# Kernel optimization log

Measured on AMD Instinct MI355X. Metric: run time of the kernel, lower is better.

## Reference

```python
import jax, jax.numpy as jnp
import numpy as np

B, S, D, H = 2, 2048, 1024, 16
HD = D // H  # 64
NUM_BUCKETS = 32
MAX_DISTANCE = 128


def _relative_position_bucket(relative_position, num_buckets=NUM_BUCKETS, max_distance=MAX_DISTANCE):
    # bidirectional=True branch of the torch code
    num_buckets //= 2
    rel_buckets = (relative_position > 0).astype(jnp.int32) * num_buckets
    rp = jnp.abs(relative_position)
    max_exact = num_buckets // 2
    is_small = rp < max_exact
    # log-spaced buckets for larger distances
    rp_large = max_exact + (
        jnp.log(rp.astype(jnp.float32) / max_exact)
        / np.log(max_distance / max_exact)
        * (num_buckets - max_exact)
    ).astype(jnp.int32)
    rp_large = jnp.minimum(rp_large, num_buckets - 1)
    return rel_buckets + jnp.where(is_small, rp, rp_large)


def compute_bias(rel_bias, query_length, key_length):
    ctx = jnp.arange(query_length)[:, None]
    mem = jnp.arange(key_length)[None, :]
    buckets = _relative_position_bucket(mem - ctx)  # [q, k]
    values = rel_bias[buckets]                      # [q, k, h]
    return jnp.transpose(values, (2, 0, 1))[None]   # [1, h, q, k]


def setup_inputs() -> dict:
    key = jax.random.key(0)
    ks = jax.random.split(key, 6)
    scale = 1.0 / np.sqrt(D)
    return {
        "hidden_states": jax.random.normal(ks[0], (B, S, D), jnp.float32),
        "mask": jnp.ones((B, 1, 1, S), jnp.int32),
        "Wq": jax.random.normal(ks[1], (D, D), jnp.float32) * scale,
        "Wk": jax.random.normal(ks[2], (D, D), jnp.float32) * scale,
        "Wv": jax.random.normal(ks[3], (D, D), jnp.float32) * scale,
        "Wo": jax.random.normal(ks[4], (D, D), jnp.float32) * scale,
        "rel_bias": jax.random.normal(ks[5], (NUM_BUCKETS, H), jnp.float32),
    }


def reference(hidden_states, mask, Wq, Wk, Wv, Wo, rel_bias):
    b, s, _ = hidden_states.shape
    # projections (no bias), split heads -> [b, h, s, hd]
    def proj(x, W):
        return jnp.einsum("bsd,ed->bse", x, W).reshape(b, s, H, HD).transpose(0, 2, 1, 3)
    q = proj(hidden_states, Wq)
    k = proj(hidden_states, Wk)
    v = proj(hidden_states, Wv)
    # unscaled attention scores (T5 style): [b, h, s, s]
    scores = jnp.einsum("bhqd,bhkd->bhqk", q, k)
    position_bias = compute_bias(rel_bias, s, s)
    scores = scores + position_bias
    scores = jnp.where(mask == 0, jnp.float32(-1e9), scores)
    attn_weights = jax.nn.softmax(scores, axis=-1)
    # dropout p=0.0 (eval): identity
    attn_output = jnp.einsum("bhqk,bhkd->bhqd", attn_weights, v)
    attn_output = attn_output.transpose(0, 2, 1, 3).reshape(b, s, H * HD)
    attn_output = jnp.einsum("bse,de->bsd", attn_output, Wo)
    return attn_output, attn_weights, position_bias
```

## Files before the change

### kernel.cpp

```cpp
#include <hip/hip_runtime.h>

typedef __attribute__((ext_vector_type(8))) _Float16 half8;
typedef __attribute__((ext_vector_type(4))) _Float16 half4;
typedef __attribute__((ext_vector_type(4))) float f32x4;

#define SEQ 2048
#define DMODEL 1024
#define NHEAD 16
#define HEADD 64
#define NBH 32
#define LUTW 4096

__device__ __forceinline__ void nt_store_f4(float* p, f32x4 v) {
    __builtin_nontemporal_store(v, (f32x4*)p);
}

#define LDS_BAR() do {                                   \
    __builtin_amdgcn_sched_barrier(0);                   \
    asm volatile("s_waitcnt lgkmcnt(0)" ::: "memory");   \
    __builtin_amdgcn_sched_barrier(0);                   \
    __builtin_amdgcn_s_barrier();                        \
    __builtin_amdgcn_sched_barrier(0);                   \
} while (0)

__device__ __forceinline__ int rel_bucket(int rel) {
    int ret = (rel > 0) ? 16 : 0;
    int rp = rel < 0 ? -rel : rel;
    if (rp < 8) return ret + rp;
    float x = logf((float)rp * 0.125f) / 2.7725887f * 8.0f;
    int v = 8 + (int)x;
    v = v < 15 ? v : 15;
    return ret + v;
}

__global__ __launch_bounds__(256) void prep_kernel(const float* __restrict__ hs,
                                                   const float* __restrict__ Wq,
                                                   const float* __restrict__ Wk,
                                                   const float* __restrict__ Wv,
                                                   const float* __restrict__ Wo,
                                                   const float* __restrict__ rel_bias,
                                                   _Float16* __restrict__ Xh,
                                                   _Float16* __restrict__ Wqh,
                                                   _Float16* __restrict__ Wkh,
                                                   _Float16* __restrict__ Wvh,
                                                   _Float16* __restrict__ Woh,
                                                   float* __restrict__ lut) {
    int bid = blockIdx.x;
    if (bid < 4096) {
        const float* in;
        _Float16* out;
        int base;
        if (bid < 2048)      { in = hs; out = Xh;  base = bid; }
        else if (bid < 2560) { in = Wq; out = Wqh; base = bid - 2048; }
        else if (bid < 3072) { in = Wk; out = Wkh; base = bid - 2560; }
        else if (bid < 3584) { in = Wv; out = Wvh; base = bid - 3072; }
        else                 { in = Wo; out = Woh; base = bid - 3584; }
        int i = (base * 256 + threadIdx.x) * 8;
        f32x4 a = *(const f32x4*)(in + i);
        f32x4 b = *(const f32x4*)(in + i + 4);
        half8 r;
        r[0] = (_Float16)a[0]; r[1] = (_Float16)a[1];
        r[2] = (_Float16)a[2]; r[3] = (_Float16)a[3];
        r[4] = (_Float16)b[0]; r[5] = (_Float16)b[1];
        r[6] = (_Float16)b[2]; r[7] = (_Float16)b[3];
        *(half8*)(out + i) = r;
    } else {
        int i = (bid - 4096) * 256 + threadIdx.x;
        int h = i >> 12;
        int idx = i & (LUTW - 1);
        int rel = idx - 2047;
        int b = rel_bucket(rel);
        lut[i] = rel_bias[b * NHEAD + h];
    }
}

__global__ __launch_bounds__(256) void proj3_kernel(const _Float16* __restrict__ Xh,
                                                    const _Float16* __restrict__ Wqh,
                                                    const _Float16* __restrict__ Wkh,
                                                    const _Float16* __restrict__ Wvh,
                                                    _Float16* __restrict__ Qh,
                                                    _Float16* __restrict__ Kh,
                                                    _Float16* __restrict__ Vt,
                                                    const float* __restrict__ lut,
                                                    float* __restrict__ posb) {
    int z = blockIdx.z;
    if (z == 3) {
        int flat = blockIdx.y * 8 + blockIdx.x;
        const size_t total = (size_t)NHEAD * SEQ * SEQ / 4;
        for (size_t idx = (size_t)flat * 256 + threadIdx.x; idx < total; idx += 65536) {
            size_t e = idx * 4;
            int k = (int)(e & 2047);
            int q = (int)((e >> 11) & 2047);
            int h = (int)(e >> 22);
            f32x4 v;
            __builtin_memcpy(&v, lut + h * LUTW + (k - q + 2047), 16);
            nt_store_f4(posb + e, v);
        }
        return;
    }
    const _Float16* B = (z == 0) ? Wqh : (z == 1) ? Wkh : Wvh;
    int l = threadIdx.x & 63, w = threadIdx.x >> 6;
    int row0 = blockIdx.y * 128 + (w >> 1) * 64;
    int col0 = blockIdx.x * 128 + (w & 1) * 64;
    int ar = l & 15, ak = (l >> 4) * 8;
    f32x4 acc[4][4] = {};
    for (int k0 = 0; k0 < DMODEL; k0 += 32) {
        half8 af[4], bf[4];
#pragma unroll
        for (int mi = 0; mi < 4; mi++)
            af[mi] = *(const half8*)(Xh + (size_t)(row0 + mi * 16 + ar) * DMODEL + k0 + ak);
#pragma unroll
        for (int ni = 0; ni < 4; ni++)
            bf[ni] = *(const half8*)(B + (size_t)(col0 + ni * 16 + ar) * DMODEL + k0 + ak);
#pragma unroll
        for (int mi = 0; mi < 4; mi++)
#pragma unroll
            for (int ni = 0; ni < 4; ni++)
                acc[mi][ni] = __builtin_amdgcn_mfma_f32_16x16x32_f16(af[mi], bf[ni], acc[mi][ni], 0, 0, 0);
    }
    int cr = (l >> 4) * 4, cc = l & 15;
    if (z < 2) {
        _Float16* C = z == 0 ? Qh : Kh;
#pragma unroll
        for (int mi = 0; mi < 4; mi++)
#pragma unroll
            for (int ni = 0; ni < 4; ni++) {
                int c = col0 + ni * 16 + cc;
#pragma unroll
                for (int j = 0; j < 4; j++)
                    C[(size_t)(row0 + mi * 16 + cr + j) * DMODEL + c] = (_Float16)acc[mi][ni][j];
            }
    } else {
#pragma unroll
        for (int mi = 0; mi < 4; mi++)
#pragma unroll
            for (int ni = 0; ni < 4; ni++) {
                int c = col0 + ni * 16 + cc;
                int h = c >> 6, hd = c & 63;
                int r = row0 + mi * 16 + cr;
                int b = r >> 11, s0 = r & 2047;
                half4 pk;
#pragma unroll
                for (int j = 0; j < 4; j++) pk[j] = (_Float16)acc[mi][ni][j];
                *(half4*)(Vt + (size_t)((b * NHEAD + h) * HEADD + hd) * SEQ + s0) = pk;
            }
    }
}

__global__ __launch_bounds__(256) void outgemm_kernel(const _Float16* __restrict__ A,
                                                      const _Float16* __restrict__ B,
                                                      float* __restrict__ C) {
    int l = threadIdx.x & 63, w = threadIdx.x >> 6;
    int row0 = blockIdx.y * 128 + (w >> 1) * 64;
    int col0 = blockIdx.x * 128 + (w & 1) * 64;
    int ar = l & 15, ak = (l >> 4) * 8;
    f32x4 acc[4][4] = {};
    for (int k0 = 0; k0 < DMODEL; k0 += 32) {
        half8 af[4], bf[4];
#pragma unroll
        for (int mi = 0; mi < 4; mi++)
            af[mi] = *(const half8*)(A + (size_t)(row0 + mi * 16 + ar) * DMODEL + k0 + ak);
#pragma unroll
        for (int ni = 0; ni < 4; ni++)
            bf[ni] = *(const half8*)(B + (size_t)(col0 + ni * 16 + ar) * DMODEL + k0 + ak);
#pragma unroll
        for (int mi = 0; mi < 4; mi++)
#pragma unroll
            for (int ni = 0; ni < 4; ni++)
                acc[mi][ni] = __builtin_amdgcn_mfma_f32_16x16x32_f16(af[mi], bf[ni], acc[mi][ni], 0, 0, 0);
    }
    int cr = (l >> 4) * 4, cc = l & 15;
#pragma unroll
    for (int mi = 0; mi < 4; mi++)
#pragma unroll
        for (int ni = 0; ni < 4; ni++) {
            int c = col0 + ni * 16 + cc;
#pragma unroll
            for (int j = 0; j < 4; j++)
                C[(size_t)(row0 + mi * 16 + cr + j) * DMODEL + c] = acc[mi][ni][j];
        }
}

__global__ __launch_bounds__(256) void attn_kernel(const _Float16* __restrict__ Q,
                                                   const _Float16* __restrict__ Kg,
                                                   const _Float16* __restrict__ Vg,
                                                   const float* __restrict__ lut,
                                                   const int* __restrict__ mask,
                                                   float* __restrict__ wts,
                                                   _Float16* __restrict__ attn0) {
    __shared__ _Float16 Kt[64][68];
    __shared__ _Float16 Vl[64][68];
    __shared__ _Float16 Pl[4][16][72];
    int tid = threadIdx.x;
    int l = tid & 63, w = tid >> 6;
    int bid = blockIdx.x;
    int xcd = bid & 7, idx = bid >> 3;
    int bh = (idx >> 4) * 8 + xcd;
    int qpair = idx & 15;
    int b = bh >> 4, h = bh & 15;
    int qbaseA = qpair * 64 + w * 16;
    int qbaseB = qbaseA + 1024;
    size_t hoff = (size_t)(b * SEQ) * DMODEL + h * HEADD;
    int ar = l & 15, g = l >> 4, ak = g * 8;
    const float* luth = lut + h * LUTW;
    float* ob = wts + (size_t)bh * SEQ * SEQ;
    int qA = qbaseA + ar;
    int qB = qbaseB + ar;

    int sr = tid >> 2, sc = (tid & 3) * 16;
    const _Float16* Ksrc = Kg + hoff + sc;
    const _Float16* Vsrc = Vg + ((size_t)bh * HEADD + sr) * SEQ + sc;

    half8 qfA[2], qfB[2];
#pragma unroll
    for (int kk = 0; kk < 2; kk++) {
        qfA[kk] = *(const half8*)(Q + hoff + (size_t)qA * DMODEL + kk * 32 + ak);
        qfB[kk] = *(const half8*)(Q + hoff + (size_t)qB * DMODEL + kk * 32 + ak);
    }

    half8 s0 = *(const half8*)(Ksrc + (size_t)sr * DMODEL);
    half8 s1 = *(const half8*)(Ksrc + (size_t)sr * DMODEL + 8);
    float mA = -3e38f, lsumA = 0.f;
    for (int k0 = 0; k0 < SEQ; k0 += 64) {
        *(half8*)&Kt[sr][sc] = s0;
        *(half8*)&Kt[sr][sc + 8] = s1;
        LDS_BAR();
        if (k0 + 64 < SEQ) {
            s0 = *(const half8*)(Ksrc + (size_t)(k0 + 64 + sr) * DMODEL);
            s1 = *(const half8*)(Ksrc + (size_t)(k0 + 64 + sr) * DMODEL + 8);
        }
        f32x4 acc[4] = {};
#pragma unroll
        for (int ni = 0; ni < 4; ni++)
#pragma unroll
            for (int kk = 0; kk < 2; kk++) {
                half8 kf = *(const half8*)&Kt[ni * 16 + ar][kk * 32 + ak];
                acc[ni] = __builtin_amdgcn_mfma_f32_16x16x32_f16(kf, qfA[kk], acc[ni], 0, 0, 0);
            }
        LDS_BAR();
        float vv[16];
#pragma unroll
        for (int ni = 0; ni < 4; ni++) {
            int kcol = k0 + ni * 16 + g * 4;
            int4 mk = *(const int4*)(mask + b * SEQ + kcol);
            const int* mp = (const int*)&mk;
            f32x4 lb4;
            __builtin_memcpy(&lb4, luth + kcol - qA + 2047, 16);
#pragma unroll
            for (int j = 0; j < 4; j++)
                vv[ni * 4 + j] = mp[j] ? (acc[ni][j] + lb4[j]) : -1e9f;
        }
        float t8[8];
#pragma unroll
        for (int t = 0; t < 8; t++) t8[t] = fmaxf(vv[t], vv[t + 8]);
        float t4a = fmaxf(t8[0], t8[4]), t4b = fmaxf(t8[1], t8[5]);
        float t4c = fmaxf(t8[2], t8[6]), t4d = fmaxf(t8[3], t8[7]);
        float vmax = fmaxf(fmaxf(t4a, t4b), fmaxf(t4c, t4d));
        float mn = fmaxf(mA, vmax);
        float scale = __expf(mA - mn);
        float e[16];
#pragma unroll
        for (int t = 0; t < 16; t++) e[t] = __expf(vv[t] - mn);
        float s8[8];
#pragma unroll
        for (int t = 0; t < 8; t++) s8[t] = e[t] + e[t + 8];
        float s4a = s8[0] + s8[4], s4b = s8[1] + s8[5];
        float s4c = s8[2] + s8[6], s4d = s8[3] + s8[7];
        lsumA = lsumA * scale + (s4a + s4b) + (s4c + s4d);
        mA = mn;
    }
    half8 t0 = *(const half8*)(Ksrc + (size_t)sr * DMODEL);
    half8 t1 = *(const half8*)(Ksrc + (size_t)sr * DMODEL + 8);
    half8 v0 = *(const half8*)(Vsrc);
    half8 v1 = *(const half8*)(Vsrc + 8);
#pragma unroll
    for (int off2 = 16; off2 <= 32; off2 <<= 1) {
        float mo = __shfl_xor(mA, off2);
        float lo = __shfl_xor(lsumA, off2);
        float mn = fmaxf(mA, mo);
        lsumA = lsumA * __expf(mA - mn) + lo * __expf(mo - mn);
        mA = mn;
    }
    float invlA = 1.0f / lsumA;
    LDS_BAR();

    f32x4 oaccA[4] = {};
    float mB = -3e38f, lsumB = 0.f;
    for (int k0 = 0; k0 < SEQ; k0 += 64) {
        *(half8*)&Kt[sr][sc] = t0;
        *(half8*)&Kt[sr][sc + 8] = t1;
        *(half8*)&Vl[sr][sc] = v0;
        *(half8*)&Vl[sr][sc + 8] = v1;
        LDS_BAR();
        if (k0 + 64 < SEQ) {
            t0 = *(const half8*)(Ksrc + (size_t)(k0 + 64 + sr) * DMODEL);
            t1 = *(const half8*)(Ksrc + (size_t)(k0 + 64 + sr) * DMODEL + 8);
            v0 = *(const half8*)(Vsrc + k0 + 64);
            v1 = *(const half8*)(Vsrc + k0 + 64 + 8);
        }
        f32x4 accA[4] = {}, accB[4] = {};
#pragma unroll
        for (int ni = 0; ni < 4; ni++)
#pragma unroll
            for (int kk = 0; kk < 2; kk++) {
                half8 kf = *(const half8*)&Kt[ni * 16 + ar][kk * 32 + ak];
                accA[ni] = __builtin_amdgcn_mfma_f32_16x16x32_f16(kf, qfA[kk], accA[ni], 0, 0, 0);
                accB[ni] = __builtin_amdgcn_mfma_f32_16x16x32_f16(kf, qfB[kk], accB[ni], 0, 0, 0);
            }
#pragma unroll
        for (int ni = 0; ni < 4; ni++) {
            int kcol = k0 + ni * 16 + g * 4;
            int4 mk = *(const int4*)(mask + b * SEQ + kcol);
            const int* mp = (const int*)&mk;
            f32x4 lb4;
            __builtin_memcpy(&lb4, luth + kcol - qA + 2047, 16);
            f32x4 wv;
#pragma unroll
            for (int j = 0; j < 4; j++) {
                float v = mp[j] ? (accA[ni][j] + lb4[j]) : -1e9f;
                wv[j] = __expf(v - mA) * invlA;
            }
            nt_store_f4(ob + (size_t)qA * SEQ + kcol, wv);
            half4 ph;
#pragma unroll
            for (int j = 0; j < 4; j++) ph[j] = (_Float16)wv[j];
            *(half4*)&Pl[w][ar][ni * 16 + g * 4] = ph;
        }
#pragma unroll
        for (int kk2 = 0; kk2 < 2; kk2++) {
            half8 pa = *(half8*)&Pl[w][ar][kk2 * 32 + g * 8];
#pragma unroll
            for (int ni = 0; ni < 4; ni++) {
                half8 vf = *(const half8*)&Vl[ni * 16 + ar][kk2 * 32 + g * 8];
                oaccA[ni] = __builtin_amdgcn_mfma_f32_16x16x32_f16(pa, vf, oaccA[ni], 0, 0, 0);
            }
        }
        {
            float vv[16];
#pragma unroll
            for (int ni = 0; ni < 4; ni++) {
                int kcol = k0 + ni * 16 + g * 4;
                int4 mk = *(const int4*)(mask + b * SEQ + kcol);
                const int* mp = (const int*)&mk;
                f32x4 lb4;
                __builtin_memcpy(&lb4, luth + kcol - qB + 2047, 16);
#pragma unroll
                for (int j = 0; j < 4; j++)
                    vv[ni * 4 + j] = mp[j] ? (accB[ni][j] + lb4[j]) : -1e9f;
            }
            float t8[8];
#pragma unroll
            for (int t = 0; t < 8; t++) t8[t] = fmaxf(vv[t], vv[t + 8]);
            float t4a = fmaxf(t8[0], t8[4]), t4b = fmaxf(t8[1], t8[5]);
            float t4c = fmaxf(t8[2], t8[6]), t4d = fmaxf(t8[3], t8[7]);
            float vmax = fmaxf(fmaxf(t4a, t4b), fmaxf(t4c, t4d));
            float mn = fmaxf(mB, vmax);
            float scale = __expf(mB - mn);
            float e[16];
#pragma unroll
            for (int t = 0; t < 16; t++) e[t] = __expf(vv[t] - mn);
            float s8[8];
#pragma unroll
            for (int t = 0; t < 8; t++) s8[t] = e[t] + e[t + 8];
            float s4a = s8[0] + s8[4], s4b = s8[1] + s8[5];
            float s4c = s8[2] + s8[6], s4d = s8[3] + s8[7];
            lsumB = lsumB * scale + (s4a + s4b) + (s4c + s4d);
            mB = mn;
        }
        LDS_BAR();
    }
#pragma unroll
    for (int ni = 0; ni < 4; ni++)
#pragma unroll
        for (int j = 0; j < 4; j++)
            attn0[(size_t)(b * SEQ + qbaseA + g * 4 + j) * DMODEL + h * HEADD + ni * 16 + ar] =
                (_Float16)oaccA[ni][j];
    half8 u0 = *(const half8*)(Ksrc + (size_t)sr * DMODEL);
    half8 u1 = *(const half8*)(Ksrc + (size_t)sr * DMODEL + 8);
    half8 w0 = *(const half8*)(Vsrc);
    half8 w1 = *(const half8*)(Vsrc + 8);
#pragma unroll
    for (int off2 = 16; off2 <= 32; off2 <<= 1) {
        float mo = __shfl_xor(mB, off2);
        float lo = __shfl_xor(lsumB, off2);
        float mn = fmaxf(mB, mo);
        lsumB = lsumB * __expf(mB - mn) + lo * __expf(mo - mn);
        mB = mn;
    }
    float invlB = 1.0f / lsumB;
    LDS_BAR();

    f32x4 oaccB[4] = {};
    for (int k0 = 0; k0 < SEQ; k0 += 64) {
        *(half8*)&Kt[sr][sc] = u0;
        *(half8*)&Kt[sr][sc + 8] = u1;
        *(half8*)&Vl[sr][sc] = w0;
        *(half8*)&Vl[sr][sc + 8] = w1;
        LDS_BAR();
        if (k0 + 64 < SEQ) {
            u0 = *(const half8*)(Ksrc + (size_t)(k0 + 64 + sr) * DMODEL);
            u1 = *(const half8*)(Ksrc + (size_t)(k0 + 64 + sr) * DMODEL + 8);
            w0 = *(const half8*)(Vsrc + k0 + 64);
            w1 = *(const half8*)(Vsrc + k0 + 64 + 8);
        }
        f32x4 acc[4] = {};
#pragma unroll
        for (int ni = 0; ni < 4; ni++)
#pragma unroll
            for (int kk = 0; kk < 2; kk++) {
                half8 kf = *(const half8*)&Kt[ni * 16 + ar][kk * 32 + ak];
                acc[ni] = __builtin_amdgcn_mfma_f32_16x16x32_f16(kf, qfB[kk], acc[ni], 0, 0, 0);
            }
#pragma unroll
        for (int ni = 0; ni < 4; ni++) {
            int kcol = k0 + ni * 16 + g * 4;
            int4 mk = *(const int4*)(mask + b * SEQ + kcol);
            const int* mp = (const int*)&mk;
            f32x4 lb4;
            __builtin_memcpy(&lb4, luth + kcol - qB + 2047, 16);
            f32x4 wv;
#pragma unroll
            for (int j = 0; j < 4; j++) {
                float v = mp[j] ? (acc[ni][j] + lb4[j]) : -1e9f;
                wv[j] = __expf(v - mB) * invlB;
            }
            nt_store_f4(ob + (size_t)qB * SEQ + kcol, wv);
            half4 ph;
#pragma unroll
            for (int j = 0; j < 4; j++) ph[j] = (_Float16)wv[j];
            *(half4*)&Pl[w][ar][ni * 16 + g * 4] = ph;
        }
#pragma unroll
        for (int kk2 = 0; kk2 < 2; kk2++) {
            half8 pa = *(half8*)&Pl[w][ar][kk2 * 32 + g * 8];
#pragma unroll
            for (int ni = 0; ni < 4; ni++) {
                half8 vf = *(const half8*)&Vl[ni * 16 + ar][kk2 * 32 + g * 8];
                oaccB[ni] = __builtin_amdgcn_mfma_f32_16x16x32_f16(pa, vf, oaccB[ni], 0, 0, 0);
            }
        }
        LDS_BAR();
    }
#pragma unroll
    for (int ni = 0; ni < 4; ni++)
#pragma unroll
        for (int j = 0; j < 4; j++)
            attn0[(size_t)(b * SEQ + qbaseB + g * 4 + j) * DMODEL + h * HEADD + ni * 16 + ar] =
                (_Float16)oaccB[ni][j];
}

extern "C" void kernel_launch(void* const* d_in, const int* in_sizes, int n_in,
                              void* d_out, int out_size, void* d_ws, size_t ws_size,
                              hipStream_t stream) {
    const float* hs = (const float*)d_in[0];
    const int* mask = (const int*)d_in[1];
    const float* Wq = (const float*)d_in[2];
    const float* Wk = (const float*)d_in[3];
    const float* Wv = (const float*)d_in[4];
    const float* Wo = (const float*)d_in[5];
    const float* rel_bias = (const float*)d_in[6];

    float* out_attn = (float*)d_out;
    float* out_wts = out_attn + (size_t)2 * SEQ * DMODEL;
    float* out_posb = out_wts + (size_t)NBH * SEQ * SEQ;

    char* ws = (char*)d_ws;
    size_t off = 0;
    auto carve = [&](size_t bytes) { void* p = ws + off; off += (bytes + 255) & ~(size_t)255; return p; };
    _Float16* Xh  = (_Float16*)carve((size_t)2 * SEQ * DMODEL * 2);
    _Float16* Wqh = (_Float16*)carve((size_t)DMODEL * DMODEL * 2);
    _Float16* Wkh = (_Float16*)carve((size_t)DMODEL * DMODEL * 2);
    _Float16* Wvh = (_Float16*)carve((size_t)DMODEL * DMODEL * 2);
    _Float16* Woh = (_Float16*)carve((size_t)DMODEL * DMODEL * 2);
    _Float16* Qh  = (_Float16*)carve((size_t)2 * SEQ * DMODEL * 2);
    _Float16* Kh  = (_Float16*)carve((size_t)2 * SEQ * DMODEL * 2);
    _Float16* Vt  = (_Float16*)carve((size_t)NBH * HEADD * SEQ * 2);
    _Float16* A0h = (_Float16*)carve((size_t)2 * SEQ * DMODEL * 2);
    float* lut    = (float*)carve((size_t)NHEAD * LUTW * 4);

    prep_kernel<<<4352, 256, 0, stream>>>(hs, Wq, Wk, Wv, Wo, rel_bias,
                                          Xh, Wqh, Wkh, Wvh, Woh, lut);

    dim3 pg(DMODEL / 128, (2 * SEQ) / 128, 4);
    proj3_kernel<<<pg, 256, 0, stream>>>(Xh, Wqh, Wkh, Wvh, Qh, Kh, Vt, lut, out_posb);

    attn_kernel<<<512, 256, 0, stream>>>(Qh, Kh, Vt, lut, mask, out_wts, A0h);

    dim3 og(DMODEL / 128, (2 * SEQ) / 128);
    outgemm_kernel<<<og, 256, 0, stream>>>(A0h, Woh, out_attn);
}
```

Measured before the change: 442.7 us.

## Double-buffer K/V tiles in LDS to halve barriers per iteration

The K and V staging tiles become two-slot LDS buffers. Each iteration now computes from the current slot, writes the prefetched next tile into the other slot, and issues a single barrier, where it previously used two. Global prefetch now runs two tiles ahead across all three passes. This cuts barrier stalls per tile at the cost of doubling the K/V LDS footprint, which may lower occupancy.

```diff
diff --git a/kernel.cpp b/kernel.cpp
--- a/kernel.cpp
+++ b/kernel.cpp
@@ -188,8 +188,8 @@
                                                    const int* __restrict__ mask,
                                                    float* __restrict__ wts,
                                                    _Float16* __restrict__ attn0) {
-    __shared__ _Float16 Kt[64][68];
-    __shared__ _Float16 Vl[64][68];
+    __shared__ _Float16 Kb[2][64][68];
+    __shared__ _Float16 Vb[2][64][68];
     __shared__ _Float16 Pl[4][16][72];
     int tid = threadIdx.x;
     int l = tid & 63, w = tid >> 6;
@@ -220,24 +220,22 @@
 
     half8 s0 = *(const half8*)(Ksrc + (size_t)sr * DMODEL);
     half8 s1 = *(const half8*)(Ksrc + (size_t)sr * DMODEL + 8);
+    *(half8*)&Kb[0][sr][sc] = s0;
+    *(half8*)&Kb[0][sr][sc + 8] = s1;
+    s0 = *(const half8*)(Ksrc + (size_t)(64 + sr) * DMODEL);
+    s1 = *(const half8*)(Ksrc + (size_t)(64 + sr) * DMODEL + 8);
+    LDS_BAR();
     float mA = -3e38f, lsumA = 0.f;
     for (int k0 = 0; k0 < SEQ; k0 += 64) {
-        *(half8*)&Kt[sr][sc] = s0;
-        *(half8*)&Kt[sr][sc + 8] = s1;
-        LDS_BAR();
-        if (k0 + 64 < SEQ) {
-            s0 = *(const half8*)(Ksrc + (size_t)(k0 + 64 + sr) * DMODEL);
-            s1 = *(const half8*)(Ksrc + (size_t)(k0 + 64 + sr) * DMODEL + 8);
-        }
+        int cur = (k0 >> 6) & 1;
         f32x4 acc[4] = {};
 #pragma unroll
         for (int ni = 0; ni < 4; ni++)
 #pragma unroll
             for (int kk = 0; kk < 2; kk++) {
-                half8 kf = *(const half8*)&Kt[ni * 16 + ar][kk * 32 + ak];
+                half8 kf = *(const half8*)&Kb[cur][ni * 16 + ar][kk * 32 + ak];
                 acc[ni] = __builtin_amdgcn_mfma_f32_16x16x32_f16(kf, qfA[kk], acc[ni], 0, 0, 0);
             }
-        LDS_BAR();
         float vv[16];
 #pragma unroll
         for (int ni = 0; ni < 4; ni++) {
@@ -268,11 +266,17 @@
         float s4c = s8[2] + s8[6], s4d = s8[3] + s8[7];
         lsumA = lsumA * scale + (s4a + s4b) + (s4c + s4d);
         mA = mn;
-    }
-    half8 t0 = *(const half8*)(Ksrc + (size_t)sr * DMODEL);
-    half8 t1 = *(const half8*)(Ksrc + (size_t)sr * DMODEL + 8);
-    half8 v0 = *(const half8*)(Vsrc);
-    half8 v1 = *(const half8*)(Vsrc + 8);
+        if (k0 + 128 < SEQ) {
+            *(half8*)&Kb[cur ^ 1][sr][sc] = s0;
+            *(half8*)&Kb[cur ^ 1][sr][sc + 8] = s1;
+            s0 = *(const half8*)(Ksrc + (size_t)(k0 + 128 + sr) * DMODEL);
+            s1 = *(const half8*)(Ksrc + (size_t)(k0 + 128 + sr) * DMODEL + 8);
+        } else if (k0 + 64 < SEQ) {
+            *(half8*)&Kb[cur ^ 1][sr][sc] = s0;
+            *(half8*)&Kb[cur ^ 1][sr][sc + 8] = s1;
+        }
+        LDS_BAR();
+    }
 #pragma unroll
     for (int off2 = 16; off2 <= 32; off2 <<= 1) {
         float mo = __shfl_xor(mA, off2);
@@ -282,28 +286,30 @@
         mA = mn;
     }
     float invlA = 1.0f / lsumA;
+
+    half8 t0 = *(const half8*)(Ksrc + (size_t)sr * DMODEL);
+    half8 t1 = *(const half8*)(Ksrc + (size_t)sr * DMODEL + 8);
+    half8 v0 = *(const half8*)(Vsrc);
+    half8 v1 = *(const half8*)(Vsrc + 8);
+    *(half8*)&Kb[0][sr][sc] = t0;
+    *(half8*)&Kb[0][sr][sc + 8] = t1;
+    *(half8*)&Vb[0][sr][sc] = v0;
+    *(half8*)&Vb[0][sr][sc + 8] = v1;
+    t0 = *(const half8*)(Ksrc + (size_t)(64 + sr) * DMODEL);
+    t1 = *(const half8*)(Ksrc + (size_t)(64 + sr) * DMODEL + 8);
+    v0 = *(const half8*)(Vsrc + 64);
+    v1 = *(const half8*)(Vsrc + 64 + 8);
     LDS_BAR();
-
     f32x4 oaccA[4] = {};
     float mB = -3e38f, lsumB = 0.f;
     for (int k0 = 0; k0 < SEQ; k0 += 64) {
-        *(half8*)&Kt[sr][sc] = t0;
-        *(half8*)&Kt[sr][sc + 8] = t1;
-        *(half8*)&Vl[sr][sc] = v0;
-        *(half8*)&Vl[sr][sc + 8] = v1;
-        LDS_BAR();
-        if (k0 + 64 < SEQ) {
-            t0 = *(const half8*)(Ksrc + (size_t)(k0 + 64 + sr) * DMODEL);
-            t1 = *(const half8*)(Ksrc + (size_t)(k0 + 64 + sr) * DMODEL + 8);
-            v0 = *(const half8*)(Vsrc + k0 + 64);
-            v1 = *(const half8*)(Vsrc + k0 + 64 + 8);
-        }
+        int cur = (k0 >> 6) & 1;
         f32x4 accA[4] = {}, accB[4] = {};
 #pragma unroll
         for (int ni = 0; ni < 4; ni++)
 #pragma unroll
             for (int kk = 0; kk < 2; kk++) {
-                half8 kf = *(const half8*)&Kt[ni * 16 + ar][kk * 32 + ak];
+                half8 kf = *(const half8*)&Kb[cur][ni * 16 + ar][kk * 32 + ak];
                 accA[ni] = __builtin_amdgcn_mfma_f32_16x16x32_f16(kf, qfA[kk], accA[ni], 0, 0, 0);
                 accB[ni] = __builtin_amdgcn_mfma_f32_16x16x32_f16(kf, qfB[kk], accB[ni], 0, 0, 0);
             }
@@ -331,7 +337,7 @@
             half8 pa = *(half8*)&Pl[w][ar][kk2 * 32 + g * 8];
 #pragma unroll
             for (int ni = 0; ni < 4; ni++) {
-                half8 vf = *(const half8*)&Vl[ni * 16 + ar][kk2 * 32 + g * 8];
+                half8 vf = *(const half8*)&Vb[cur][ni * 16 + ar][kk2 * 32 + g * 8];
                 oaccA[ni] = __builtin_amdgcn_mfma_f32_16x16x32_f16(pa, vf, oaccA[ni], 0, 0, 0);
             }
         }
@@ -367,6 +373,21 @@
             lsumB = lsumB * scale + (s4a + s4b) + (s4c + s4d);
             mB = mn;
         }
+        if (k0 + 128 < SEQ) {
+            *(half8*)&Kb[cur ^ 1][sr][sc] = t0;
+            *(half8*)&Kb[cur ^ 1][sr][sc + 8] = t1;
+            *(half8*)&Vb[cur ^ 1][sr][sc] = v0;
+            *(half8*)&Vb[cur ^ 1][sr][sc + 8] = v1;
+            t0 = *(const half8*)(Ksrc + (size_t)(k0 + 128 + sr) * DMODEL);
+            t1 = *(const half8*)(Ksrc + (size_t)(k0 + 128 + sr) * DMODEL + 8);
+            v0 = *(const half8*)(Vsrc + k0 + 128);
+            v1 = *(const half8*)(Vsrc + k0 + 128 + 8);
+        } else if (k0 + 64 < SEQ) {
+            *(half8*)&Kb[cur ^ 1][sr][sc] = t0;
+            *(half8*)&Kb[cur ^ 1][sr][sc + 8] = t1;
+            *(half8*)&Vb[cur ^ 1][sr][sc] = v0;
+            *(half8*)&Vb[cur ^ 1][sr][sc + 8] = v1;
+        }
         LDS_BAR();
     }
 #pragma unroll
@@ -375,10 +396,6 @@
         for (int j = 0; j < 4; j++)
             attn0[(size_t)(b * SEQ + qbaseA + g * 4 + j) * DMODEL + h * HEADD + ni * 16 + ar] =
                 (_Float16)oaccA[ni][j];
-    half8 u0 = *(const half8*)(Ksrc + (size_t)sr * DMODEL);
-    half8 u1 = *(const half8*)(Ksrc + (size_t)sr * DMODEL + 8);
-    half8 w0 = *(const half8*)(Vsrc);
-    half8 w1 = *(const half8*)(Vsrc + 8);
 #pragma unroll
     for (int off2 = 16; off2 <= 32; off2 <<= 1) {
         float mo = __shfl_xor(mB, off2);
@@ -388,27 +405,29 @@
         mB = mn;
     }
     float invlB = 1.0f / lsumB;
+
+    half8 u0 = *(const half8*)(Ksrc + (size_t)sr * DMODEL);
+    half8 u1 = *(const half8*)(Ksrc + (size_t)sr * DMODEL + 8);
+    half8 w0 = *(const half8*)(Vsrc);
+    half8 w1 = *(const half8*)(Vsrc + 8);
+    *(half8*)&Kb[0][sr][sc] = u0;
+    *(half8*)&Kb[0][sr][sc + 8] = u1;
+    *(half8*)&Vb[0][sr][sc] = w0;
+    *(half8*)&Vb[0][sr][sc + 8] = w1;
+    u0 = *(const half8*)(Ksrc + (size_t)(64 + sr) * DMODEL);
+    u1 = *(const half8*)(Ksrc + (size_t)(64 + sr) * DMODEL + 8);
+    w0 = *(const half8*)(Vsrc + 64);
+    w1 = *(const half8*)(Vsrc + 64 + 8);
     LDS_BAR();
-
     f32x4 oaccB[4] = {};
     for (int k0 = 0; k0 < SEQ; k0 += 64) {
-        *(half8*)&Kt[sr][sc] = u0;
-        *(half8*)&Kt[sr][sc + 8] = u1;
-        *(half8*)&Vl[sr][sc] = w0;
-        *(half8*)&Vl[sr][sc + 8] = w1;
-        LDS_BAR();
-        if (k0 + 64 < SEQ) {
-            u0 = *(const half8*)(Ksrc + (size_t)(k0 + 64 + sr) * DMODEL);
-            u1 = *(const half8*)(Ksrc + (size_t)(k0 + 64 + sr) * DMODEL + 8);
-            w0 = *(const half8*)(Vsrc + k0 + 64);
-            w1 = *(const half8*)(Vsrc + k0 + 64 + 8);
-        }
+        int cur = (k0 >> 6) & 1;
         f32x4 acc[4] = {};
 #pragma unroll
         for (int ni = 0; ni < 4; ni++)
 #pragma unroll
             for (int kk = 0; kk < 2; kk++) {
-                half8 kf = *(const half8*)&Kt[ni * 16 + ar][kk * 32 + ak];
+                half8 kf = *(const half8*)&Kb[cur][ni * 16 + ar][kk * 32 + ak];
                 acc[ni] = __builtin_amdgcn_mfma_f32_16x16x32_f16(kf, qfB[kk], acc[ni], 0, 0, 0);
             }
 #pragma unroll
@@ -435,9 +454,24 @@
             half8 pa = *(half8*)&Pl[w][ar][kk2 * 32 + g * 8];
 #pragma unroll
             for (int ni = 0; ni < 4; ni++) {
-                half8 vf = *(const half8*)&Vl[ni * 16 + ar][kk2 * 32 + g * 8];
+                half8 vf = *(const half8*)&Vb[cur][ni * 16 + ar][kk2 * 32 + g * 8];
                 oaccB[ni] = __builtin_amdgcn_mfma_f32_16x16x32_f16(pa, vf, oaccB[ni], 0, 0, 0);
             }
+        }
+        if (k0 + 128 < SEQ) {
+            *(half8*)&Kb[cur ^ 1][sr][sc] = u0;
+            *(half8*)&Kb[cur ^ 1][sr][sc + 8] = u1;
+            *(half8*)&Vb[cur ^ 1][sr][sc] = w0;
+            *(half8*)&Vb[cur ^ 1][sr][sc + 8] = w1;
+            u0 = *(const half8*)(Ksrc + (size_t)(k0 + 128 + sr) * DMODEL);
+            u1 = *(const half8*)(Ksrc + (size_t)(k0 + 128 + sr) * DMODEL + 8);
+            w0 = *(const half8*)(Vsrc + k0 + 128);
+            w1 = *(const half8*)(Vsrc + k0 + 128 + 8);
+        } else if (k0 + 64 < SEQ) {
+            *(half8*)&Kb[cur ^ 1][sr][sc] = u0;
+            *(half8*)&Kb[cur ^ 1][sr][sc + 8] = u1;
+            *(half8*)&Vb[cur ^ 1][sr][sc] = w0;
+            *(half8*)&Vb[cur ^ 1][sr][sc + 8] = w1;
         }
         LDS_BAR();
     }
```

Measured after the change: 447.5 us. No clear change (+1.1%).

## Merge row-stat passes for both query tiles, drop third K/V sweep

Applied to the files above, without the earlier changes.

The first K sweep now computes the running softmax max and sum for both query tiles A and B at once, with the cross-lane reductions done together. The second sweep then writes normalized weights and accumulates P·V for both tiles, so the separate third sweep over K/V for tile B is removed. This cuts one full pass of K/V global loads, LDS staging and barriers per block. In exchange, two output accumulator sets and more softmax state stay live at the same time, which raises register pressure and may lower occupancy.

```diff
diff --git a/kernel.cpp b/kernel.cpp
--- a/kernel.cpp
+++ b/kernel.cpp
@@ -221,6 +221,7 @@
     half8 s0 = *(const half8*)(Ksrc + (size_t)sr * DMODEL);
     half8 s1 = *(const half8*)(Ksrc + (size_t)sr * DMODEL + 8);
     float mA = -3e38f, lsumA = 0.f;
+    float mB = -3e38f, lsumB = 0.f;
     for (int k0 = 0; k0 < SEQ; k0 += 64) {
         *(half8*)&Kt[sr][sc] = s0;
         *(half8*)&Kt[sr][sc + 8] = s1;
@@ -229,45 +230,80 @@
             s0 = *(const half8*)(Ksrc + (size_t)(k0 + 64 + sr) * DMODEL);
             s1 = *(const half8*)(Ksrc + (size_t)(k0 + 64 + sr) * DMODEL + 8);
         }
-        f32x4 acc[4] = {};
+        f32x4 accA[4] = {}, accB[4] = {};
 #pragma unroll
         for (int ni = 0; ni < 4; ni++)
 #pragma unroll
             for (int kk = 0; kk < 2; kk++) {
                 half8 kf = *(const half8*)&Kt[ni * 16 + ar][kk * 32 + ak];
-                acc[ni] = __builtin_amdgcn_mfma_f32_16x16x32_f16(kf, qfA[kk], acc[ni], 0, 0, 0);
+                accA[ni] = __builtin_amdgcn_mfma_f32_16x16x32_f16(kf, qfA[kk], accA[ni], 0, 0, 0);
+                accB[ni] = __builtin_amdgcn_mfma_f32_16x16x32_f16(kf, qfB[kk], accB[ni], 0, 0, 0);
             }
         LDS_BAR();
-        float vv[16];
-#pragma unroll
-        for (int ni = 0; ni < 4; ni++) {
-            int kcol = k0 + ni * 16 + g * 4;
-            int4 mk = *(const int4*)(mask + b * SEQ + kcol);
-            const int* mp = (const int*)&mk;
-            f32x4 lb4;
-            __builtin_memcpy(&lb4, luth + kcol - qA + 2047, 16);
-#pragma unroll
-            for (int j = 0; j < 4; j++)
-                vv[ni * 4 + j] = mp[j] ? (acc[ni][j] + lb4[j]) : -1e9f;
-        }
-        float t8[8];
-#pragma unroll
-        for (int t = 0; t < 8; t++) t8[t] = fmaxf(vv[t], vv[t + 8]);
-        float t4a = fmaxf(t8[0], t8[4]), t4b = fmaxf(t8[1], t8[5]);
-        float t4c = fmaxf(t8[2], t8[6]), t4d = fmaxf(t8[3], t8[7]);
-        float vmax = fmaxf(fmaxf(t4a, t4b), fmaxf(t4c, t4d));
-        float mn = fmaxf(mA, vmax);
-        float scale = __expf(mA - mn);
-        float e[16];
-#pragma unroll
-        for (int t = 0; t < 16; t++) e[t] = __expf(vv[t] - mn);
-        float s8[8];
-#pragma unroll
-        for (int t = 0; t < 8; t++) s8[t] = e[t] + e[t + 8];
-        float s4a = s8[0] + s8[4], s4b = s8[1] + s8[5];
-        float s4c = s8[2] + s8[6], s4d = s8[3] + s8[7];
-        lsumA = lsumA * scale + (s4a + s4b) + (s4c + s4d);
-        mA = mn;
+        {
+            float vv[16];
+#pragma unroll
+            for (int ni = 0; ni < 4; ni++) {
+                int kcol = k0 + ni * 16 + g * 4;
+                int4 mk = *(const int4*)(mask + b * SEQ + kcol);
+                const int* mp = (const int*)&mk;
+                f32x4 lb4;
+                __builtin_memcpy(&lb4, luth + kcol - qA + 2047, 16);
+#pragma unroll
+                for (int j = 0; j < 4; j++)
+                    vv[ni * 4 + j] = mp[j] ? (accA[ni][j] + lb4[j]) : -1e9f;
+            }
+            float t8[8];
+#pragma unroll
+            for (int t = 0; t < 8; t++) t8[t] = fmaxf(vv[t], vv[t + 8]);
+            float t4a = fmaxf(t8[0], t8[4]), t4b = fmaxf(t8[1], t8[5]);
+            float t4c = fmaxf(t8[2], t8[6]), t4d = fmaxf(t8[3], t8[7]);
+            float vmax = fmaxf(fmaxf(t4a, t4b), fmaxf(t4c, t4d));
+            float mn = fmaxf(mA, vmax);
+            float scale = __expf(mA - mn);
+            float e[16];
+#pragma unroll
+            for (int t = 0; t < 16; t++) e[t] = __expf(vv[t] - mn);
+            float s8[8];
+#pragma unroll
+            for (int t = 0; t < 8; t++) s8[t] = e[t] + e[t + 8];
+            float s4a = s8[0] + s8[4], s4b = s8[1] + s8[5];
+            float s4c = s8[2] + s8[6], s4d = s8[3] + s8[7];
+            lsumA = lsumA * scale + (s4a + s4b) + (s4c + s4d);
+            mA = mn;
+        }
+        {
+            float vv[16];
+#pragma unroll
+            for (int ni = 0; ni < 4; ni++) {
+                int kcol = k0 + ni * 16 + g * 4;
+                int4 mk = *(const int4*)(mask + b * SEQ + kcol);
+                const int* mp = (const int*)&mk;
+                f32x4 lb4;
+                __builtin_memcpy(&lb4, luth + kcol - qB + 2047, 16);
+#pragma unroll
+                for (int j = 0; j < 4; j++)
+                    vv[ni * 4 + j] = mp[j] ? (accB[ni][j] + lb4[j]) : -1e9f;
+            }
+            float t8[8];
+#pragma unroll
+            for (int t = 0; t < 8; t++) t8[t] = fmaxf(vv[t], vv[t + 8]);
+            float t4a = fmaxf(t8[0], t8[4]), t4b = fmaxf(t8[1], t8[5]);
+            float t4c = fmaxf(t8[2], t8[6]), t4d = fmaxf(t8[3], t8[7]);
+            float vmax = fmaxf(fmaxf(t4a, t4b), fmaxf(t4c, t4d));
+            float mn = fmaxf(mB, vmax);
+            float scale = __expf(mB - mn);
+            float e[16];
+#pragma unroll
+            for (int t = 0; t < 16; t++) e[t] = __expf(vv[t] - mn);
+            float s8[8];
+#pragma unroll
+            for (int t = 0; t < 8; t++) s8[t] = e[t] + e[t + 8];
+            float s4a = s8[0] + s8[4], s4b = s8[1] + s8[5];
+            float s4c = s8[2] + s8[6], s4d = s8[3] + s8[7];
+            lsumB = lsumB * scale + (s4a + s4b) + (s4c + s4d);
+            mB = mn;
+        }
     }
     half8 t0 = *(const half8*)(Ksrc + (size_t)sr * DMODEL);
     half8 t1 = *(const half8*)(Ksrc + (size_t)sr * DMODEL + 8);
@@ -280,12 +316,17 @@
         float mn = fmaxf(mA, mo);
         lsumA = lsumA * __expf(mA - mn) + lo * __expf(mo - mn);
         mA = mn;
+        mo = __shfl_xor(mB, off2);
+        lo = __shfl_xor(lsumB, off2);
+        mn = fmaxf(mB, mo);
+        lsumB = lsumB * __expf(mB - mn) + lo * __expf(mo - mn);
+        mB = mn;
     }
     float invlA = 1.0f / lsumA;
+    float invlB = 1.0f / lsumB;
     LDS_BAR();
 
-    f32x4 oaccA[4] = {};
-    float mB = -3e38f, lsumB = 0.f;
+    f32x4 oaccA[4] = {}, oaccB[4] = {};
     for (int k0 = 0; k0 < SEQ; k0 += 64) {
         *(half8*)&Kt[sr][sc] = t0;
         *(half8*)&Kt[sr][sc + 8] = t1;
@@ -335,82 +376,6 @@
                 oaccA[ni] = __builtin_amdgcn_mfma_f32_16x16x32_f16(pa, vf, oaccA[ni], 0, 0, 0);
             }
         }
-        {
-            float vv[16];
-#pragma unroll
-            for (int ni = 0; ni < 4; ni++) {
-                int kcol = k0 + ni * 16 + g * 4;
-                int4 mk = *(const int4*)(mask + b * SEQ + kcol);
-                const int* mp = (const int*)&mk;
-                f32x4 lb4;
-                __builtin_memcpy(&lb4, luth + kcol - qB + 2047, 16);
-#pragma unroll
-                for (int j = 0; j < 4; j++)
-                    vv[ni * 4 + j] = mp[j] ? (accB[ni][j] + lb4[j]) : -1e9f;
-            }
-            float t8[8];
-#pragma unroll
-            for (int t = 0; t < 8; t++) t8[t] = fmaxf(vv[t], vv[t + 8]);
-            float t4a = fmaxf(t8[0], t8[4]), t4b = fmaxf(t8[1], t8[5]);
-            float t4c = fmaxf(t8[2], t8[6]), t4d = fmaxf(t8[3], t8[7]);
-            float vmax = fmaxf(fmaxf(t4a, t4b), fmaxf(t4c, t4d));
-            float mn = fmaxf(mB, vmax);
-            float scale = __expf(mB - mn);
-            float e[16];
-#pragma unroll
-            for (int t = 0; t < 16; t++) e[t] = __expf(vv[t] - mn);
-            float s8[8];
-#pragma unroll
-            for (int t = 0; t < 8; t++) s8[t] = e[t] + e[t + 8];
-            float s4a = s8[0] + s8[4], s4b = s8[1] + s8[5];
-            float s4c = s8[2] + s8[6], s4d = s8[3] + s8[7];
-            lsumB = lsumB * scale + (s4a + s4b) + (s4c + s4d);
-            mB = mn;
-        }
-        LDS_BAR();
-    }
-#pragma unroll
-    for (int ni = 0; ni < 4; ni++)
-#pragma unroll
-        for (int j = 0; j < 4; j++)
-            attn0[(size_t)(b * SEQ + qbaseA + g * 4 + j) * DMODEL + h * HEADD + ni * 16 + ar] =
-                (_Float16)oaccA[ni][j];
-    half8 u0 = *(const half8*)(Ksrc + (size_t)sr * DMODEL);
-    half8 u1 = *(const half8*)(Ksrc + (size_t)sr * DMODEL + 8);
-    half8 w0 = *(const half8*)(Vsrc);
-    half8 w1 = *(const half8*)(Vsrc + 8);
-#pragma unroll
-    for (int off2 = 16; off2 <= 32; off2 <<= 1) {
-        float mo = __shfl_xor(mB, off2);
-        float lo = __shfl_xor(lsumB, off2);
-        float mn = fmaxf(mB, mo);
-        lsumB = lsumB * __expf(mB - mn) + lo * __expf(mo - mn);
-        mB = mn;
-    }
-    float invlB = 1.0f / lsumB;
-    LDS_BAR();
-
-    f32x4 oaccB[4] = {};
-    for (int k0 = 0; k0 < SEQ; k0 += 64) {
-        *(half8*)&Kt[sr][sc] = u0;
-        *(half8*)&Kt[sr][sc + 8] = u1;
-        *(half8*)&Vl[sr][sc] = w0;
-        *(half8*)&Vl[sr][sc + 8] = w1;
-        LDS_BAR();
-        if (k0 + 64 < SEQ) {
-            u0 = *(const half8*)(Ksrc + (size_t)(k0 + 64 + sr) * DMODEL);
-            u1 = *(const half8*)(Ksrc + (size_t)(k0 + 64 + sr) * DMODEL + 8);
-            w0 = *(const half8*)(Vsrc + k0 + 64);
-            w1 = *(const half8*)(Vsrc + k0 + 64 + 8);
-        }
-        f32x4 acc[4] = {};
-#pragma unroll
-        for (int ni = 0; ni < 4; ni++)
-#pragma unroll
-            for (int kk = 0; kk < 2; kk++) {
-                half8 kf = *(const half8*)&Kt[ni * 16 + ar][kk * 32 + ak];
-                acc[ni] = __builtin_amdgcn_mfma_f32_16x16x32_f16(kf, qfB[kk], acc[ni], 0, 0, 0);
-            }
 #pragma unroll
         for (int ni = 0; ni < 4; ni++) {
             int kcol = k0 + ni * 16 + g * 4;
@@ -421,7 +386,7 @@
             f32x4 wv;
 #pragma unroll
             for (int j = 0; j < 4; j++) {
-                float v = mp[j] ? (acc[ni][j] + lb4[j]) : -1e9f;
+                float v = mp[j] ? (accB[ni][j] + lb4[j]) : -1e9f;
                 wv[j] = __expf(v - mB) * invlB;
             }
             nt_store_f4(ob + (size_t)qB * SEQ + kcol, wv);
@@ -444,9 +409,12 @@
 #pragma unroll
     for (int ni = 0; ni < 4; ni++)
 #pragma unroll
-        for (int j = 0; j < 4; j++)
+        for (int j = 0; j < 4; j++) {
+            attn0[(size_t)(b * SEQ + qbaseA + g * 4 + j) * DMODEL + h * HEADD + ni * 16 + ar] =
+                (_Float16)oaccA[ni][j];
             attn0[(size_t)(b * SEQ + qbaseB + g * 4 + j) * DMODEL + h * HEADD + ni * 16 + ar] =
                 (_Float16)oaccB[ni][j];
+        }
 }
 
 extern "C" void kernel_launch(void* const* d_in, const int* in_sizes, int n_in,
```

New measurement: 433.6 us. 1.02x faster.
